# Kernel optimization log

Measured on AMD Instinct MI355X. Metric: run time of the kernel, lower is better.

## Reference

```python
import jax, jax.numpy as jnp
import numpy as np

N, E, G = 50000, 600000, 64
F_NODE, F_EDGE, F_HAD = 20, 4, 12
D, H, C, L = 128, 4, 32, 3  # hidden, heads, per-head channels, num_layers


def setup_inputs() -> dict:
    key = jax.random.key(0)
    ks = iter(jax.random.split(key, 64))
    nrm = lambda shp, s=0.1: jax.random.normal(next(ks), shp, dtype=jnp.float32) * s
    inp = {
        'x': jax.random.normal(next(ks), (N, F_NODE), dtype=jnp.float32),
        'edge_attr': jax.random.normal(next(ks), (E, F_EDGE), dtype=jnp.float32),
        'haddock_features': jax.random.normal(next(ks), (G, F_HAD), dtype=jnp.float32),
        'edge_index': jax.random.randint(next(ks), (2, E), 0, N, dtype=jnp.int64),
        'batch': (jnp.arange(N, dtype=jnp.int64) * G) // N,  # sorted, all graphs non-empty
        # node embed
        'embed_w': nrm((F_NODE, D)), 'embed_b': jnp.zeros((D,), jnp.float32),
        # GAT layers (stacked over L)
        'gat_lin_w': nrm((L, D, H * C)),
        'gat_att_src': nrm((L, H, C)), 'gat_att_dst': nrm((L, H, C)),
        'gat_edge_w': nrm((L, F_EDGE, H * C)), 'gat_att_edge': nrm((L, H, C)),
        'gat_bias': jnp.zeros((L, H * C), jnp.float32),
        'ln_g': jnp.ones((L, D), jnp.float32), 'ln_b': jnp.zeros((L, D), jnp.float32),
        # haddock processor
        'had_w1': nrm((F_HAD, D)), 'had_b1': jnp.zeros((D,), jnp.float32),
        'had_w2': nrm((D, D)), 'had_b2': jnp.zeros((D,), jnp.float32),
        # interaction head (in = 3*D)
        'int_w1': nrm((3 * D, D)), 'int_b1': jnp.zeros((D,), jnp.float32),
        'int_w2': nrm((D, 64)), 'int_b2': jnp.zeros((64,), jnp.float32),
        'int_w3': nrm((64, 1)), 'int_b3': jnp.zeros((1,), jnp.float32),
        # binding affinity head
        'aff_w1': nrm((3 * D, D)), 'aff_b1': jnp.zeros((D,), jnp.float32),
        'aff_w2': nrm((D, 64)), 'aff_b2': jnp.zeros((64,), jnp.float32),
        'aff_w3': nrm((64, 1)), 'aff_b3': jnp.zeros((1,), jnp.float32),
        # MultiheadAttention with seq_len=1: softmax over 1 key == 1, so output
        # reduces exactly to out_proj(v_proj(x)); q/k projections cancel.
        'mha_v_w': nrm((D, D)), 'mha_v_b': jnp.zeros((D,), jnp.float32),
        'mha_o_w': nrm((D, D)), 'mha_o_b': jnp.zeros((D,), jnp.float32),
    }
    return inp


def _layernorm(x, g, b, eps=1e-5):
    mu = jnp.mean(x, axis=-1, keepdims=True)
    var = jnp.var(x, axis=-1, keepdims=True)
    return (x - mu) * jax.lax.rsqrt(var + eps) * g + b


def _gat_layer(x, src, dst, edge_attr, lin_w, a_src, a_dst, edge_w, a_edge, bias):
    n = x.shape[0]
    h = (x @ lin_w).reshape(n, H, C)                      # [N,H,C]
    alpha_s = jnp.sum(h * a_src, axis=-1)                 # [N,H]
    alpha_d = jnp.sum(h * a_dst, axis=-1)                 # [N,H]
    eemb = (edge_attr @ edge_w).reshape(-1, H, C)         # [E,H,C]
    alpha_e = jnp.sum(eemb * a_edge, axis=-1)             # [E,H]
    alpha = alpha_s[src] + alpha_d[dst] + alpha_e         # [E,H]
    alpha = jax.nn.leaky_relu(alpha, 0.2)
    m = jax.ops.segment_max(alpha, dst, num_segments=n)
    m = jnp.where(jnp.isfinite(m), m, 0.0)
    ex = jnp.exp(alpha - m[dst])
    denom = jax.ops.segment_sum(ex, dst, num_segments=n)
    w = ex / (denom[dst] + 1e-16)                         # segment softmax over dst
    msg = h[src] * w[:, :, None]                          # [E,H,C]
    out = jax.ops.segment_sum(msg, dst, num_segments=n)   # [N,H,C]
    return out.reshape(n, H * C) + bias


def reference(x, edge_attr, haddock_features, embed_w, embed_b,
              gat_lin_w, gat_att_src, gat_att_dst, gat_edge_w, gat_att_edge, gat_bias,
              ln_g, ln_b, had_w1, had_b1, had_w2, had_b2,
              int_w1, int_b1, int_w2, int_b2, int_w3, int_b3,
              aff_w1, aff_b1, aff_w2, aff_b2, aff_w3, aff_b3,
              mha_v_w, mha_v_b, mha_o_w, mha_o_b, edge_index, batch):
    src, dst = edge_index[0], edge_index[1]
    h = jax.nn.relu(x @ embed_w + embed_b)
    for i in range(L):
        res = h
        h = _gat_layer(h, src, dst, edge_attr, gat_lin_w[i], gat_att_src[i],
                       gat_att_dst[i], gat_edge_w[i], gat_att_edge[i], gat_bias[i])
        h = jax.nn.relu(_layernorm(h + res, ln_g[i], ln_b[i]))  # dropout = identity (eval)
    counts = jax.ops.segment_sum(jnp.ones((h.shape[0],), h.dtype), batch, num_segments=G)
    g_mean = jax.ops.segment_sum(h, batch, num_segments=G) / counts[:, None]
    g_max = jax.ops.segment_max(h, batch, num_segments=G)
    graph_embed = jnp.concatenate([g_mean, g_max], axis=1)      # [G,2D]
    had = jax.nn.relu(haddock_features @ had_w1 + had_b1) @ had_w2 + had_b2
    comb = jnp.concatenate([graph_embed, had], axis=1)          # [G,3D]
    z = jax.nn.relu(comb @ int_w1 + int_b1)
    z = jax.nn.relu(z @ int_w2 + int_b2)
    interaction = jax.nn.sigmoid(z @ int_w3 + int_b3)[:, 0]
    z = jax.nn.relu(comb @ aff_w1 + aff_b1)
    z = jax.nn.relu(z @ aff_w2 + aff_b2)
    affinity = (z @ aff_w3 + aff_b3)[:, 0]
    # self-attention over seq_len=1: weights==1, output = out_proj(v_proj(x))
    attn = (h @ mha_v_w + mha_v_b) @ mha_o_w + mha_o_b
    return interaction, affinity, attn, h
```

## Files before the change

### kernel.cpp

```cpp
#include <hip/hip_runtime.h>
#include <hip/hip_bf16.h>

typedef float v4 __attribute__((ext_vector_type(4)));
typedef float f32x4 __attribute__((ext_vector_type(4)));
typedef short bf16x8 __attribute__((ext_vector_type(8)));
typedef unsigned short us8 __attribute__((ext_vector_type(8)));

__device__ __forceinline__ unsigned short f2bf(float f) {
    unsigned u = __float_as_uint(f);
    u = (u + 0x7FFFu + ((u >> 16) & 1u)) >> 16;
    return (unsigned short)u;
}
__device__ __forceinline__ float bf2f(unsigned short s) {
    return __uint_as_float(((unsigned)s) << 16);
}

__global__ __launch_bounds__(256) void k_embed(const float* __restrict__ x,
                                               const float* __restrict__ w,
                                               const float* __restrict__ b,
                                               unsigned short* __restrict__ h_bf, int n) {
    int idx = blockIdx.x * 256 + threadIdx.x;
    if (idx >= n * 128) return;
    int node = idx >> 7, j = idx & 127;
    float acc = b[j];
#pragma unroll
    for (int k = 0; k < 20; ++k) acc += x[node * 20 + k] * w[k * 128 + j];
    h_bf[idx] = f2bf(fmaxf(acc, 0.f));
}


__global__ __launch_bounds__(256) void k_hist(const int* __restrict__ ei,
                                              int* __restrict__ cnt, int E_) {
    int e = blockIdx.x * 256 + threadIdx.x;
    if (e < E_) atomicAdd(&cnt[ei[E_ + e]], 1);
}

__global__ __launch_bounds__(256) void k_scan_local(const int* __restrict__ cnt,
                                                    int* __restrict__ ptr,
                                                    int* __restrict__ bsum, int n) {
    __shared__ int s[256];
    int t = threadIdx.x, i = blockIdx.x * 256 + t;
    int v = (i < n) ? cnt[i] : 0;
    s[t] = v;
    __syncthreads();
    for (int o = 1; o < 256; o <<= 1) {
        int x = (t >= o) ? s[t - o] : 0;
        __syncthreads();
        s[t] += x;
        __syncthreads();
    }
    if (i < n) ptr[i] = s[t] - v;
    if (t == 255) bsum[blockIdx.x] = s[255];
}

__global__ __launch_bounds__(256) void k_scan_bsum(int* __restrict__ bsum, int nb) {
    __shared__ int s[256];
    int t = threadIdx.x;
    int v = (t < nb) ? bsum[t] : 0;
    s[t] = v;
    __syncthreads();
    for (int o = 1; o < 256; o <<= 1) {
        int x = (t >= o) ? s[t - o] : 0;
        __syncthreads();
        s[t] += x;
        __syncthreads();
    }
    if (t < nb) bsum[t] = s[t] - v;
}

__global__ __launch_bounds__(256) void k_scan_add(int* __restrict__ ptr,
                                                  const int* __restrict__ bsum,
                                                  int n, int E_) {
    int i = blockIdx.x * 256 + threadIdx.x;
    if (i < n) ptr[i] += bsum[i >> 8];
    if (i == 0) ptr[n] = E_;
}

__global__ __launch_bounds__(256) void k_scatter(const int* __restrict__ ei,
                                                 const float* __restrict__ edge_attr,
                                                 const int* __restrict__ ptr,
                                                 int* __restrict__ cursor,
                                                 int* __restrict__ esrc_s,
                                                 float* __restrict__ ea_s, int E_) {
    int e = blockIdx.x * 256 + threadIdx.x;
    if (e >= E_) return;
    int d = ei[E_ + e];
    int p = ptr[d] + atomicAdd(&cursor[d], 1);
    esrc_s[p] = ei[e];
    ((v4*)ea_s)[p] = ((const v4*)edge_attr)[e];
}

__global__ __launch_bounds__(128) void k_fuse_vo(const float* __restrict__ vw,
                                                 const float* __restrict__ vb,
                                                 const float* __restrict__ ow,
                                                 const float* __restrict__ ob,
                                                 float* __restrict__ Wc,
                                                 float* __restrict__ bc) {
    int k = blockIdx.x, j = threadIdx.x;
    float acc = 0.f;
    for (int m = 0; m < 128; ++m) acc += vw[k * 128 + m] * ow[m * 128 + j];
    Wc[k * 128 + j] = acc;
    if (k == 0) {
        float b = ob[j];
        for (int m = 0; m < 128; ++m) b += vb[m] * ow[m * 128 + j];
        bc[j] = b;
    }
}

__global__ __launch_bounds__(256) void k_pack_w(const float* __restrict__ gat_lin_w,
                                                const float* __restrict__ Wc,
                                                unsigned short* __restrict__ Bpack) {
    int m = blockIdx.y;
    const float* W = (m < 3) ? (gat_lin_w + (size_t)m * 16384) : Wc;
    int idx = blockIdx.x * 256 + threadIdx.x;
    int e = idx & 7, l = (idx >> 3) & 63, kb = (idx >> 9) & 3, c = idx >> 11;
    int k = kb * 32 + ((l >> 4) << 3) + e;
    int col = c * 16 + (l & 15);
    Bpack[(size_t)m * 16384 + idx] = f2bf(W[k * 128 + col]);
}

template <bool ALPHAS, bool OUTF32>
__global__ __launch_bounds__(256) void k_gemm_mfma(
    const unsigned short* __restrict__ A,
    const unsigned short* __restrict__ Bpack,
    const float* __restrict__ bias,
    unsigned short* __restrict__ out_bf,
    float* __restrict__ out_f32,
    const float* __restrict__ avs, const float* __restrict__ avd,
    float* __restrict__ asrc, float* __restrict__ adst, int nn) {
    __shared__ float lds[64][132];
    int tid = threadIdx.x;
    int w = tid >> 6, l = tid & 63;
    int row0 = blockIdx.x * 64;
    int arow = row0 + w * 16 + (l & 15);
    int koff = (l >> 4) * 8;

    bf16x8 a[4];
#pragma unroll
    for (int kb = 0; kb < 4; ++kb)
        a[kb] = *(const bf16x8*)&A[(size_t)arow * 128 + kb * 32 + koff];

    const bf16x8* bp = (const bf16x8*)Bpack;
    f32x4 acc[8];
#pragma unroll
    for (int c = 0; c < 8; ++c) {
        f32x4 z = {0.f, 0.f, 0.f, 0.f};
        acc[c] = z;
#pragma unroll
        for (int kb = 0; kb < 4; ++kb)
            acc[c] = __builtin_amdgcn_mfma_f32_16x16x32_bf16(a[kb], bp[(c * 4 + kb) * 64 + l],
                                                             acc[c], 0, 0, 0);
    }

    int colb = l & 15;
    int rowb = w * 16 + (l >> 4) * 4;
#pragma unroll
    for (int c = 0; c < 8; ++c)
#pragma unroll
        for (int r = 0; r < 4; ++r)
            lds[rowb + r][c * 16 + colb] = acc[c][r];
    __syncthreads();

    int rl = tid >> 2, q = tid & 3;
    int gr = row0 + rl;
    if (gr >= nn) return;
    float v[32];
#pragma unroll
    for (int j = 0; j < 8; ++j)
        *(f32x4*)&v[j * 4] = *(const f32x4*)&lds[rl][q * 32 + j * 4];

    if (ALPHAS) {
        float ps = 0.f, pd = 0.f;
#pragma unroll
        for (int j = 0; j < 32; ++j) {
            ps += v[j] * avs[q * 32 + j];
            pd += v[j] * avd[q * 32 + j];
        }
        asrc[(size_t)gr * 4 + q] = ps;
        adst[(size_t)gr * 4 + q] = pd;
    }
    if (OUTF32) {
#pragma unroll
        for (int j = 0; j < 32; ++j) v[j] += bias[q * 32 + j];
#pragma unroll
        for (int j = 0; j < 8; ++j)
            *(f32x4*)&out_f32[(size_t)gr * 128 + q * 32 + j * 4] = *(f32x4*)&v[j * 4];
    } else {
        us8 o[4];
#pragma unroll
        for (int t = 0; t < 4; ++t)
#pragma unroll
            for (int j = 0; j < 8; ++j) o[t][j] = f2bf(v[t * 8 + j]);
#pragma unroll
        for (int t = 0; t < 4; ++t)
            *(us8*)&out_bf[(size_t)gr * 128 + q * 32 + t * 8] = o[t];
    }
}

template <bool LAST>
__global__ __launch_bounds__(256) void k_node_agg(
    const unsigned short* __restrict__ hl_bf, const int* __restrict__ ptr,
    const int* __restrict__ esrc_s, const float* __restrict__ ea_s,
    const float* __restrict__ asrc, const float* __restrict__ adst,
    const float* __restrict__ edge_w, const float* __restrict__ a_edge,
    const float* __restrict__ bias, const float* __restrict__ lng,
    const float* __restrict__ lnb, float* __restrict__ h_f32,
    unsigned short* __restrict__ h_bf, int n) {
    __shared__ float aew[16];
    int tid = threadIdx.x;
    if (tid < 16) {
        int k = tid >> 2, hh = tid & 3;
        float s = 0.f;
        for (int c = 0; c < 32; ++c) s += edge_w[k * 128 + hh * 32 + c] * a_edge[hh * 32 + c];
        aew[tid] = s;
    }
    __syncthreads();

    int node = blockIdx.x * 4 + (tid >> 6);
    if (node >= n) return;
    int lane = tid & 63;
    int g = lane >> 4;
    int l16 = lane & 15;
    int c0 = l16 * 8;
    int hh = l16 >> 2;

    float aewc0 = aew[hh], aewc1 = aew[4 + hh], aewc2 = aew[8 + hh], aewc3 = aew[12 + hh];
    int start = ptr[node], end = ptr[node + 1];
    float adn = adst[(size_t)node * 4 + hh];
    us8 res_bf = *(const us8*)&h_bf[(size_t)node * 128 + c0];

    float acc[8] = {};
    float den = 0.f;
    int p = start + g;
    int srcp = (p < end) ? esrc_s[p] : 0;
    for (; p < end; p += 4) {
        int srcn = (p + 4 < end) ? esrc_s[p + 4] : 0;
        v4 ea = ((const v4*)ea_s)[p];
        float a = asrc[(size_t)srcp * 4 + hh] + adn +
                  ea[0] * aewc0 + ea[1] * aewc1 + ea[2] * aewc2 + ea[3] * aewc3;
        a = a > 0.f ? a : 0.2f * a;
        float ex = __expf(a);
        den += ex;
        us8 hv = *(const us8*)&hl_bf[(size_t)srcp * 128 + c0];
#pragma unroll
        for (int j = 0; j < 8; ++j) acc[j] += ex * bf2f(hv[j]);
        srcp = srcn;
    }

#pragma unroll
    for (int j = 0; j < 8; ++j) {
        acc[j] += __shfl_xor(acc[j], 16);
        acc[j] += __shfl_xor(acc[j], 32);
    }
    den += __shfl_xor(den, 16);
    den += __shfl_xor(den, 32);

    float inv = 1.f / (den + 1e-16f);
    v4 b0 = *(const v4*)&bias[c0];
    v4 b1 = *(const v4*)&bias[c0 + 4];
    float v[8];
#pragma unroll
    for (int j = 0; j < 4; ++j) v[j] = acc[j] * inv + b0[j] + bf2f(res_bf[j]);
#pragma unroll
    for (int j = 0; j < 4; ++j) v[4 + j] = acc[4 + j] * inv + b1[j] + bf2f(res_bf[4 + j]);

    float s = 0.f, sq = 0.f;
#pragma unroll
    for (int j = 0; j < 8; ++j) { s += v[j]; sq += v[j] * v[j]; }
#pragma unroll
    for (int o = 1; o < 16; o <<= 1) { s += __shfl_xor(s, o); sq += __shfl_xor(sq, o); }
    float mu = s * (1.f / 128.f);
    float var = sq * (1.f / 128.f) - mu * mu;
    float rs = rsqrtf(var + 1e-5f);

    if (g == 0) {
        v4 g0 = *(const v4*)&lng[c0];
        v4 g1 = *(const v4*)&lng[c0 + 4];
        v4 lb0 = *(const v4*)&lnb[c0];
        v4 lb1 = *(const v4*)&lnb[c0 + 4];
        v4 o0, o1;
#pragma unroll
        for (int j = 0; j < 4; ++j) o0[j] = fmaxf((v[j] - mu) * rs * g0[j] + lb0[j], 0.f);
#pragma unroll
        for (int j = 0; j < 4; ++j) o1[j] = fmaxf((v[4 + j] - mu) * rs * g1[j] + lb1[j], 0.f);
        us8 ob;
#pragma unroll
        for (int j = 0; j < 4; ++j) ob[j] = f2bf(o0[j]);
#pragma unroll
        for (int j = 0; j < 4; ++j) ob[4 + j] = f2bf(o1[j]);
        *(us8*)&h_bf[(size_t)node * 128 + c0] = ob;
        if (LAST) {
            *(v4*)&h_f32[(size_t)node * 128 + c0] = o0;
            *(v4*)&h_f32[(size_t)node * 128 + c0 + 4] = o1;
        }
    }
}

__device__ __forceinline__ int lower_bound_i(const int* a, int n, int key) {
    int lo = 0, hi = n;
    while (lo < hi) {
        int mid = (lo + hi) >> 1;
        if (a[mid] < key) lo = mid + 1; else hi = mid;
    }
    return lo;
}


__global__ __launch_bounds__(256) void k_pool_part(const unsigned short* __restrict__ h_bf,
                                                   const int* __restrict__ batch,
                                                   float* __restrict__ gsum,
                                                   float* __restrict__ gmax,
                                                   int n, int chunk) {
    int start = blockIdx.x * chunk;
    int end = min(start + chunk, n);
    if (start >= end) return;
    int c0 = (threadIdx.x & 63) * 2;
    int strm = threadIdx.x >> 6;
    float s0 = 0.f, s1 = 0.f, m0 = 0.f, m1 = 0.f;
    int curg = -1;
    for (int node = start + strm; node < end; node += 4) {
        int g = batch[node];
        if (g != curg) {
            if (curg >= 0) {
                atomicAdd(&gsum[curg * 128 + c0], s0);
                atomicAdd(&gsum[curg * 128 + c0 + 1], s1);
                atomicMax((int*)&gmax[curg * 128 + c0], __float_as_int(m0));
                atomicMax((int*)&gmax[curg * 128 + c0 + 1], __float_as_int(m1));
            }
            curg = g; s0 = s1 = 0.f; m0 = m1 = 0.f;
        }
        unsigned u = *(const unsigned*)&h_bf[(size_t)node * 128 + c0];
        float v0 = __uint_as_float(u << 16);
        float v1 = __uint_as_float(u & 0xffff0000u);
        s0 += v0; s1 += v1;
        m0 = fmaxf(m0, v0); m1 = fmaxf(m1, v1);
    }
    if (curg >= 0) {
        atomicAdd(&gsum[curg * 128 + c0], s0);
        atomicAdd(&gsum[curg * 128 + c0 + 1], s1);
        atomicMax((int*)&gmax[curg * 128 + c0], __float_as_int(m0));
        atomicMax((int*)&gmax[curg * 128 + c0 + 1], __float_as_int(m1));
    }
}

__global__ __launch_bounds__(256) void k_graph_out(
    const float* __restrict__ gsum, const float* __restrict__ gmax,
    const int* __restrict__ batch, const float* __restrict__ hf,
    const float* __restrict__ had_w1, const float* __restrict__ had_b1,
    const float* __restrict__ had_w2, const float* __restrict__ had_b2,
    const float* __restrict__ int_w1, const float* __restrict__ int_b1,
    const float* __restrict__ int_w2, const float* __restrict__ int_b2,
    const float* __restrict__ int_w3, const float* __restrict__ int_b3,
    const float* __restrict__ aff_w1, const float* __restrict__ aff_b1,
    const float* __restrict__ aff_w2, const float* __restrict__ aff_b2,
    const float* __restrict__ aff_w3, const float* __restrict__ aff_b3,
    float* __restrict__ inter_out, float* __restrict__ aff_out, int n) {
    __shared__ float comb[384];
    __shared__ float h1[128];
    __shared__ float z1[2][128];
    __shared__ float z2[2][64];
    int g = blockIdx.x, tid = threadIdx.x;
    if (tid < 128) {
        int start = lower_bound_i(batch, n, g);
        int end = lower_bound_i(batch, n, g + 1);
        float cnt = (float)(end - start);
        comb[tid] = gsum[g * 128 + tid] / cnt;
        comb[128 + tid] = gmax[g * 128 + tid];
        float acc = had_b1[tid];
#pragma unroll
        for (int k = 0; k < 12; ++k) acc += hf[g * 12 + k] * had_w1[k * 128 + tid];
        h1[tid] = fmaxf(acc, 0.f);
    }
    __syncthreads();
    if (tid < 128) {
        float a2 = had_b2[tid];
        for (int k = 0; k < 128; ++k) a2 += h1[k] * had_w2[k * 128 + tid];
        comb[256 + tid] = a2;
    }
    __syncthreads();
    int hsel = tid >> 7, j = tid & 127;
    const float* w1 = hsel ? aff_w1 : int_w1;
    const float* b1 = hsel ? aff_b1 : int_b1;
    const float* w2 = hsel ? aff_w2 : int_w2;
    const float* b2 = hsel ? aff_b2 : int_b2;
    const float* w3 = hsel ? aff_w3 : int_w3;
    const float* b3 = hsel ? aff_b3 : int_b3;
    float acc = b1[j];
    for (int k = 0; k < 384; ++k) acc += comb[k] * w1[k * 128 + j];
    z1[hsel][j] = fmaxf(acc, 0.f);
    __syncthreads();
    if (j < 64) {
        float a2 = b2[j];
        for (int k = 0; k < 128; ++k) a2 += z1[hsel][k] * w2[k * 64 + j];
        z2[hsel][j] = fmaxf(a2, 0.f);
    }
    __syncthreads();
    if (j == 0) {
        float a3 = b3[0];
        for (int k = 0; k < 64; ++k) a3 += z2[hsel][k] * w3[k];
        if (hsel) aff_out[g] = a3;
        else inter_out[g] = 1.f / (1.f + __expf(-a3));
    }
}

extern "C" void kernel_launch(void* const* d_in, const int* in_sizes, int n_in,
                              void* d_out, int out_size, void* d_ws, size_t ws_size,
                              hipStream_t stream) {
    const float* x = (const float*)d_in[0];
    const float* edge_attr = (const float*)d_in[1];
    const float* haddock = (const float*)d_in[2];
    const int* ei = (const int*)d_in[3];
    const int* batch = (const int*)d_in[4];
    const float* embed_w = (const float*)d_in[5];
    const float* embed_b = (const float*)d_in[6];
    const float* gat_lin_w = (const float*)d_in[7];
    const float* gat_att_src = (const float*)d_in[8];
    const float* gat_att_dst = (const float*)d_in[9];
    const float* gat_edge_w = (const float*)d_in[10];
    const float* gat_att_edge = (const float*)d_in[11];
    const float* gat_bias = (const float*)d_in[12];
    const float* ln_g = (const float*)d_in[13];
    const float* ln_b = (const float*)d_in[14];
    const float* had_w1 = (const float*)d_in[15];
    const float* had_b1 = (const float*)d_in[16];
    const float* had_w2 = (const float*)d_in[17];
    const float* had_b2 = (const float*)d_in[18];
    const float* int_w1 = (const float*)d_in[19];
    const float* int_b1 = (const float*)d_in[20];
    const float* int_w2 = (const float*)d_in[21];
    const float* int_b2 = (const float*)d_in[22];
    const float* int_w3 = (const float*)d_in[23];
    const float* int_b3 = (const float*)d_in[24];
    const float* aff_w1 = (const float*)d_in[25];
    const float* aff_b1 = (const float*)d_in[26];
    const float* aff_w2 = (const float*)d_in[27];
    const float* aff_b2 = (const float*)d_in[28];
    const float* aff_w3 = (const float*)d_in[29];
    const float* aff_b3 = (const float*)d_in[30];
    const float* mha_v_w = (const float*)d_in[31];
    const float* mha_v_b = (const float*)d_in[32];
    const float* mha_o_w = (const float*)d_in[33];
    const float* mha_o_b = (const float*)d_in[34];

    const int N_ = in_sizes[0] / 20;
    const int E_ = in_sizes[1] / 4;
    const int G_ = in_sizes[2] / 12;
    const int Npad = (N_ + 63) & ~63;

    float* out_f = (float*)d_out;
    float* inter_out = out_f;
    float* aff_out = out_f + G_;
    float* attn_out = out_f + 2 * G_;
    float* h_buf = attn_out + (size_t)N_ * 128;

    unsigned short* h_bf = (unsigned short*)d_ws;
    unsigned short* hl_bf = h_bf + (size_t)Npad * 128;
    unsigned short* Bpack = hl_bf + (size_t)Npad * 128;
    float* ea_s = (float*)(Bpack + 4 * 16384);
    float* Wc = ea_s + (size_t)E_ * 4;
    float* bc = Wc + 16384;
    float* asrc = bc + 128;
    float* adst = asrc + (size_t)N_ * 4;
    float* gsum = adst + (size_t)N_ * 4;
    float* gmax = gsum + (size_t)G_ * 128;
    int* cnt = (int*)(gmax + (size_t)G_ * 128);
    int* cursor = cnt + N_;
    int* ptr = cursor + N_;
    int* bsum = ptr + N_ + 4;
    int* esrc_s = bsum + 256;

    const int nb_scan = (N_ + 255) / 256;
    const int POOL_BLOCKS = 2048;
    const int chunk = (N_ + POOL_BLOCKS - 1) / POOL_BLOCKS;
    const int gemm_blocks = (N_ + 63) / 64;

    k_embed<<<(N_ * 128 + 255) / 256, 256, 0, stream>>>(x, embed_w, embed_b, h_bf, N_);

    hipMemsetAsync(cnt, 0, (size_t)2 * N_ * sizeof(int), stream);
    k_hist<<<(E_ + 255) / 256, 256, 0, stream>>>(ei, cnt, E_);
    k_scan_local<<<nb_scan, 256, 0, stream>>>(cnt, ptr, bsum, N_);
    k_scan_bsum<<<1, 256, 0, stream>>>(bsum, nb_scan);
    k_scan_add<<<nb_scan, 256, 0, stream>>>(ptr, bsum, N_, E_);
    k_scatter<<<(E_ + 255) / 256, 256, 0, stream>>>(ei, edge_attr, ptr, cursor,
                                                    esrc_s, ea_s, E_);

    k_fuse_vo<<<128, 128, 0, stream>>>(mha_v_w, mha_v_b, mha_o_w, mha_o_b, Wc, bc);
    k_pack_w<<<dim3(64, 4), 256, 0, stream>>>(gat_lin_w, Wc, Bpack);
    hipMemsetAsync(gsum, 0, (size_t)2 * G_ * 128 * sizeof(float), stream);

    for (int i = 0; i < 3; ++i) {
        k_gemm_mfma<true, false><<<gemm_blocks, 256, 0, stream>>>(
            h_bf, Bpack + (size_t)i * 16384, nullptr, hl_bf, nullptr,
            gat_att_src + i * 128, gat_att_dst + i * 128, asrc, adst, N_);
        if (i < 2)
            k_node_agg<false><<<(N_ + 3) / 4, 256, 0, stream>>>(
                hl_bf, ptr, esrc_s, ea_s, asrc, adst,
                gat_edge_w + (size_t)i * 512, gat_att_edge + i * 128,
                gat_bias + i * 128, ln_g + i * 128, ln_b + i * 128, h_buf, h_bf, N_);
        else
            k_node_agg<true><<<(N_ + 3) / 4, 256, 0, stream>>>(
                hl_bf, ptr, esrc_s, ea_s, asrc, adst,
                gat_edge_w + (size_t)i * 512, gat_att_edge + i * 128,
                gat_bias + i * 128, ln_g + i * 128, ln_b + i * 128, h_buf, h_bf, N_);
    }

    k_pool_part<<<POOL_BLOCKS, 256, 0, stream>>>(h_bf, batch, gsum, gmax, N_, chunk);
    k_graph_out<<<G_, 256, 0, stream>>>(gsum, gmax, batch, haddock,
                                        had_w1, had_b1, had_w2, had_b2,
                                        int_w1, int_b1, int_w2, int_b2, int_w3, int_b3,
                                        aff_w1, aff_b1, aff_w2, aff_b2, aff_w3, aff_b3,
                                        inter_out, aff_out, N_);
    k_gemm_mfma<false, true><<<gemm_blocks, 256, 0, stream>>>(
        h_bf, Bpack + (size_t)3 * 16384, bc, nullptr, attn_out,
        nullptr, nullptr, nullptr, nullptr, N_);
}
```

Baseline: 394.3 us.

## Pad CSR segments to 4 and batch gathers with shuffled attention weights

```diff
diff --git a/kernel.cpp b/kernel.cpp
--- a/kernel.cpp
+++ b/kernel.cpp
@@ -5,6 +5,7 @@
 typedef float f32x4 __attribute__((ext_vector_type(4)));
 typedef short bf16x8 __attribute__((ext_vector_type(8)));
 typedef unsigned short us8 __attribute__((ext_vector_type(8)));
+typedef unsigned short us4 __attribute__((ext_vector_type(4)));
 
 __device__ __forceinline__ unsigned short f2bf(float f) {
     unsigned u = __float_as_uint(f);
@@ -40,7 +41,7 @@
                                                     int* __restrict__ bsum, int n) {
     __shared__ int s[256];
     int t = threadIdx.x, i = blockIdx.x * 256 + t;
-    int v = (i < n) ? cnt[i] : 0;
+    int v = (i < n) ? ((cnt[i] + 3) & ~3) : 0;
     s[t] = v;
     __syncthreads();
     for (int o = 1; o < 256; o <<= 1) {
@@ -69,11 +70,9 @@
 }
 
 __global__ __launch_bounds__(256) void k_scan_add(int* __restrict__ ptr,
-                                                  const int* __restrict__ bsum,
-                                                  int n, int E_) {
+                                                  const int* __restrict__ bsum, int n) {
     int i = blockIdx.x * 256 + threadIdx.x;
     if (i < n) ptr[i] += bsum[i >> 8];
-    if (i == 0) ptr[n] = E_;
 }
 
 __global__ __launch_bounds__(256) void k_scatter(const int* __restrict__ ei,
@@ -81,13 +80,17 @@
                                                  const int* __restrict__ ptr,
                                                  int* __restrict__ cursor,
                                                  int* __restrict__ esrc_s,
-                                                 float* __restrict__ ea_s, int E_) {
+                                                 unsigned short* __restrict__ ea_s, int E_) {
     int e = blockIdx.x * 256 + threadIdx.x;
     if (e >= E_) return;
     int d = ei[E_ + e];
     int p = ptr[d] + atomicAdd(&cursor[d], 1);
     esrc_s[p] = ei[e];
-    ((v4*)ea_s)[p] = ((const v4*)edge_attr)[e];
+    v4 ea = ((const v4*)edge_attr)[e];
+    us4 o;
+#pragma unroll
+    for (int j = 0; j < 4; ++j) o[j] = f2bf(ea[j]);
+    *(us4*)&ea_s[(size_t)p * 4] = o;
 }
 
 __global__ __launch_bounds__(128) void k_fuse_vo(const float* __restrict__ vw,
@@ -200,7 +203,8 @@
 template <bool LAST>
 __global__ __launch_bounds__(256) void k_node_agg(
     const unsigned short* __restrict__ hl_bf, const int* __restrict__ ptr,
-    const int* __restrict__ esrc_s, const float* __restrict__ ea_s,
+    const int* __restrict__ cnt,
+    const int* __restrict__ esrc_s, const unsigned short* __restrict__ ea_s,
     const float* __restrict__ asrc, const float* __restrict__ adst,
     const float* __restrict__ edge_w, const float* __restrict__ a_edge,
     const float* __restrict__ bias, const float* __restrict__ lng,
@@ -221,30 +225,48 @@
     int lane = tid & 63;
     int g = lane >> 4;
     int l16 = lane & 15;
+    int hh = l16 >> 2;
+    int q = l16 & 3;
     int c0 = l16 * 8;
-    int hh = l16 >> 2;
+    int lb = lane & ~3;
 
     float aewc0 = aew[hh], aewc1 = aew[4 + hh], aewc2 = aew[8 + hh], aewc3 = aew[12 + hh];
-    int start = ptr[node], end = ptr[node + 1];
+    int start = ptr[node];
+    int end = start + cnt[node];
     float adn = adst[(size_t)node * 4 + hh];
     us8 res_bf = *(const us8*)&h_bf[(size_t)node * 128 + c0];
 
     float acc[8] = {};
     float den = 0.f;
-    int p = start + g;
-    int srcp = (p < end) ? esrc_s[p] : 0;
-    for (; p < end; p += 4) {
-        int srcn = (p + 4 < end) ? esrc_s[p + 4] : 0;
-        v4 ea = ((const v4*)ea_s)[p];
-        float a = asrc[(size_t)srcp * 4 + hh] + adn +
-                  ea[0] * aewc0 + ea[1] * aewc1 + ea[2] * aewc2 + ea[3] * aewc3;
+    for (int base = start + g * 4; base < end; base += 16) {
+        int4 s4 = *(const int4*)&esrc_s[base];
+        bool val = (base + q) < end;
+        int eaidx = val ? (base + q) : start;
+        us4 eab = *(const us4*)&ea_s[(size_t)eaidx * 4];
+        int se = (q == 0) ? s4.x : (q == 1) ? s4.y : (q == 2) ? s4.z : s4.w;
+        se = val ? se : 0;
+        float a = asrc[(size_t)se * 4 + hh] + adn +
+                  bf2f(eab[0]) * aewc0 + bf2f(eab[1]) * aewc1 +
+                  bf2f(eab[2]) * aewc2 + bf2f(eab[3]) * aewc3;
         a = a > 0.f ? a : 0.2f * a;
-        float ex = __expf(a);
-        den += ex;
-        us8 hv = *(const us8*)&hl_bf[(size_t)srcp * 128 + c0];
-#pragma unroll
-        for (int j = 0; j < 8; ++j) acc[j] += ex * bf2f(hv[j]);
-        srcp = srcn;
+        float exo = val ? __expf(a) : 0.f;
+        int su0 = (base + 0 < end) ? s4.x : 0;
+        int su1 = (base + 1 < end) ? s4.y : 0;
+        int su2 = (base + 2 < end) ? s4.z : 0;
+        int su3 = (base + 3 < end) ? s4.w : 0;
+        us8 hv0 = *(const us8*)&hl_bf[(size_t)su0 * 128 + c0];
+        us8 hv1 = *(const us8*)&hl_bf[(size_t)su1 * 128 + c0];
+        us8 hv2 = *(const us8*)&hl_bf[(size_t)su2 * 128 + c0];
+        us8 hv3 = *(const us8*)&hl_bf[(size_t)su3 * 128 + c0];
+        float ex0 = __shfl(exo, lb);
+        float ex1 = __shfl(exo, lb + 1);
+        float ex2 = __shfl(exo, lb + 2);
+        float ex3 = __shfl(exo, lb + 3);
+        den += (ex0 + ex1) + (ex2 + ex3);
+#pragma unroll
+        for (int j = 0; j < 8; ++j)
+            acc[j] += ex0 * bf2f(hv0[j]) + ex1 * bf2f(hv1[j]) +
+                      ex2 * bf2f(hv2[j]) + ex3 * bf2f(hv3[j]);
     }
 
 #pragma unroll
@@ -446,6 +468,7 @@
     const int E_ = in_sizes[1] / 4;
     const int G_ = in_sizes[2] / 12;
     const int Npad = (N_ + 63) & ~63;
+    const int Epad = E_ + 4 * N_ + 16;
 
     float* out_f = (float*)d_out;
     float* inter_out = out_f;
@@ -456,8 +479,8 @@
     unsigned short* h_bf = (unsigned short*)d_ws;
     unsigned short* hl_bf = h_bf + (size_t)Npad * 128;
     unsigned short* Bpack = hl_bf + (size_t)Npad * 128;
-    float* ea_s = (float*)(Bpack + 4 * 16384);
-    float* Wc = ea_s + (size_t)E_ * 4;
+    unsigned short* ea_s = Bpack + 4 * 16384;
+    float* Wc = (float*)(ea_s + (size_t)Epad * 4);
     float* bc = Wc + 16384;
     float* asrc = bc + 128;
     float* adst = asrc + (size_t)N_ * 4;
@@ -480,7 +503,7 @@
     k_hist<<<(E_ + 255) / 256, 256, 0, stream>>>(ei, cnt, E_);
     k_scan_local<<<nb_scan, 256, 0, stream>>>(cnt, ptr, bsum, N_);
     k_scan_bsum<<<1, 256, 0, stream>>>(bsum, nb_scan);
-    k_scan_add<<<nb_scan, 256, 0, stream>>>(ptr, bsum, N_, E_);
+    k_scan_add<<<nb_scan, 256, 0, stream>>>(ptr, bsum, N_);
     k_scatter<<<(E_ + 255) / 256, 256, 0, stream>>>(ei, edge_attr, ptr, cursor,
                                                     esrc_s, ea_s, E_);
 
@@ -494,12 +517,12 @@
             gat_att_src + i * 128, gat_att_dst + i * 128, asrc, adst, N_);
         if (i < 2)
             k_node_agg<false><<<(N_ + 3) / 4, 256, 0, stream>>>(
-                hl_bf, ptr, esrc_s, ea_s, asrc, adst,
+                hl_bf, ptr, cnt, esrc_s, ea_s, asrc, adst,
                 gat_edge_w + (size_t)i * 512, gat_att_edge + i * 128,
                 gat_bias + i * 128, ln_g + i * 128, ln_b + i * 128, h_buf, h_bf, N_);
         else
             k_node_agg<true><<<(N_ + 3) / 4, 256, 0, stream>>>(
-                hl_bf, ptr, esrc_s, ea_s, asrc, adst,
+                hl_bf, ptr, cnt, esrc_s, ea_s, asrc, adst,
                 gat_edge_w + (size_t)i * 512, gat_att_edge + i * 128,
                 gat_bias + i * 128, ln_g + i * 128, ln_b + i * 128, h_buf, h_bf, N_);
     }
```

New measurement: 419.4 us. +6.4%, slower.
